# Optimization experiments

Measured on AMD Instinct MI355X. Metric: run time of the kernel, lower is better.

Reference implementation:

```python
import jax, jax.numpy as jnp
import numpy as np

B, S, HID = 1, 2048, 2048
NH = 16
D_NOPE, D_ROPE, D_V = 128, 64, 128
D_QK = D_NOPE + D_ROPE            # 192
KV_R = 512                        # kv_lora_rank
EPS = 1e-6
SCALING = D_QK ** -0.5
NEG = -1e9


def rms_norm(x, w):
    xf = x.astype(jnp.float32)
    var = jnp.mean(xf * xf, axis=-1, keepdims=True)
    return w * (xf * jax.lax.rsqrt(var + EPS)).astype(x.dtype)


def rotate_half(x):
    x1, x2 = jnp.split(x, 2, axis=-1)
    return jnp.concatenate([-x2, x1], axis=-1)


def deinterleave(x):
    # torch: view(..., d//2, 2).transpose(-1, -2).reshape(..., d)
    # => [x0, x2, x4, ..., x1, x3, x5, ...]
    return jnp.concatenate([x[..., 0::2], x[..., 1::2]], axis=-1)


def setup_inputs() -> dict:
    key = jax.random.key(0)
    ks = jax.random.split(key, 6)
    hidden_states = jax.random.normal(ks[0], (B, S, HID), jnp.float32)
    # rotary cos/sin over qk_rope_head_dim
    inv_freq = 1.0 / (10000.0 ** (np.arange(0, D_ROPE, 2, dtype=np.float32) / D_ROPE))
    freqs = np.outer(np.arange(S, dtype=np.float32), inv_freq)   # [S, D_ROPE/2]
    emb = np.concatenate([freqs, freqs], axis=-1)                # [S, D_ROPE]
    cos = jnp.asarray(np.cos(emb), jnp.float32)[None]            # [1, S, D_ROPE]
    sin = jnp.asarray(np.sin(emb), jnp.float32)[None]
    # additive causal mask [1, 1, S, S]
    causal = np.where(np.tril(np.ones((S, S), dtype=bool)), 0.0, NEG).astype(np.float32)
    attention_mask = jnp.asarray(causal)[None, None]
    sc = lambda k, shp: jax.random.normal(k, shp, jnp.float32) * (shp[-1] ** -0.5)
    q_proj_w = sc(ks[1], (NH * D_QK, HID))
    kv_a_proj_w = sc(ks[2], (KV_R + D_ROPE, HID))
    kv_a_ln_w = jnp.ones((KV_R,), jnp.float32)
    kv_b_proj_w = sc(ks[3], (NH * (D_NOPE + D_V), KV_R))
    o_proj_w = sc(ks[4], (HID, NH * D_V))
    return dict(hidden_states=hidden_states, cos=cos, sin=sin,
                attention_mask=attention_mask, q_proj_w=q_proj_w,
                kv_a_proj_w=kv_a_proj_w, kv_a_ln_w=kv_a_ln_w,
                kv_b_proj_w=kv_b_proj_w, o_proj_w=o_proj_w)


def reference(hidden_states, cos, sin, attention_mask,
              q_proj_w, kv_a_proj_w, kv_a_ln_w, kv_b_proj_w, o_proj_w):
    b, s, _ = hidden_states.shape
    # Q projection -> [b, NH, s, D_QK]
    q = (hidden_states @ q_proj_w.T).reshape(b, s, NH, D_QK).transpose(0, 2, 1, 3)
    q_pass, q_rot = q[..., :D_NOPE], q[..., D_NOPE:]
    # compressed KV + shared rope key
    ckv = hidden_states @ kv_a_proj_w.T                           # [b, s, KV_R + D_ROPE]
    k_pass_c, k_rot = ckv[..., :KV_R], ckv[..., KV_R:]
    kv = (rms_norm(k_pass_c, kv_a_ln_w) @ kv_b_proj_w.T)
    kv = kv.reshape(b, s, NH, D_NOPE + D_V).transpose(0, 2, 1, 3)  # [b, NH, s, .]
    k_pass, value_states = kv[..., :D_NOPE], kv[..., D_NOPE:]
    k_rot = k_rot.reshape(b, 1, s, D_ROPE)
    # interleaved RoPE (rope_interleave=True)
    q_rot = deinterleave(q_rot)
    k_rot = deinterleave(k_rot)
    c = cos[:, None]  # [1, 1, s, D_ROPE]
    sn = sin[:, None]
    q_rot = q_rot * c + rotate_half(q_rot) * sn
    k_rot = k_rot * c + rotate_half(k_rot) * sn
    k_rot = jnp.broadcast_to(k_rot, (b, NH, s, D_ROPE))
    query_states = jnp.concatenate([q_pass, q_rot], axis=-1)      # [b, NH, s, D_QK]
    key_states = jnp.concatenate([k_pass, k_rot], axis=-1)
    # eager attention (num_key_value_groups == 1)
    scores = jnp.einsum('bhqd,bhkd->bhqk', query_states, key_states) * SCALING
    scores = scores + attention_mask[:, :, :, :s]
    attn = jax.nn.softmax(scores.astype(jnp.float32), axis=-1).astype(query_states.dtype)
    attn_out = jnp.einsum('bhqk,bhkd->bhqd', attn, value_states)  # [b, NH, s, D_V]
    attn_out = attn_out.transpose(0, 2, 1, 3).reshape(b, s, NH * D_V)
    return attn_out @ o_proj_w.T
```

## Files before the change

kernel.cpp:

```cpp
#include <hip/hip_runtime.h>
#include <hip/hip_bf16.h>
#include <stdint.h>
#include <stddef.h>

#define S_LEN 2048
#define HID_DIM 2048
#define NH 16
#define D_QK 192
#define D_NOPE 128
#define D_ROPE 64
#define D_V 128
#define KV_R 512
#define CKV_N (KV_R + D_ROPE)
#define KVB_N (NH * (D_NOPE + D_V))
#define QN (NH * D_QK)
#define SCALING 0.07216878364870322f

typedef __attribute__((ext_vector_type(8))) short short8;
typedef __attribute__((ext_vector_type(4))) short short4v;
typedef __attribute__((ext_vector_type(4))) float f32x4;

__device__ __forceinline__ short f2bf_bits(float f) {
  unsigned u = __float_as_uint(f);
  unsigned r = (u + 0x7fffu + ((u >> 16) & 1u)) >> 16;
  return (short)(r & 0xffffu);
}
__device__ __forceinline__ float bf2f(short b) {
  return __uint_as_float(((unsigned)(unsigned short)b) << 16);
}

__device__ __forceinline__ f32x4 mfma_bf16(short8 a, short8 b, f32x4 c) {
  return __builtin_amdgcn_mfma_f32_16x16x32_bf16(a, b, c, 0, 0, 0);
}

__global__ __launch_bounds__(256)
void cvt_k(const float* __restrict__ in, short* __restrict__ out, int n4) {
  const int i = blockIdx.x * 256 + threadIdx.x;
  if (i >= n4) return;
  const float4 v = ((const float4*)in)[i];
  short4v o;
  o.x = f2bf_bits(v.x); o.y = f2bf_bits(v.y);
  o.z = f2bf_bits(v.z); o.w = f2bf_bits(v.w);
  ((short4v*)out)[i] = o;
}

template <bool OUTF32>
__global__ __launch_bounds__(256, 3)
void gemm_bt(const short* __restrict__ A, const short* __restrict__ B,
             void* __restrict__ Cv, int M, int N, int K) {
  __shared__ short sA[2][128 * 32];
  __shared__ short sB[2][128 * 32];
  const int tid  = threadIdx.x;
  const int wave = tid >> 6;
  const int lane = tid & 63;
  const int bm = blockIdx.y * 128;
  const int bn = blockIdx.x * 128;
  const int wr = wave >> 1, wc = wave & 1;
  const int fr = lane & 15, fk = (lane >> 4) * 8;
  const int srow = lane >> 2;
  const int scol = (lane & 3) * 8;

  f32x4 acc[4][4];
  for (int i = 0; i < 4; ++i)
    for (int j = 0; j < 4; ++j)
      for (int r = 0; r < 4; ++r) acc[i][j][r] = 0.f;

  for (int k0 = 0; k0 < K; k0 += 64) {
    __syncthreads();
#pragma unroll
    for (int cc = 0; cc < 2; ++cc) {
      const int c = wave * 2 + cc;
      const int ar = bm + c * 16 + srow;
      int br = bn + c * 16 + srow; if (br > N - 1) br = N - 1;
#pragma unroll
      for (int kh = 0; kh < 2; ++kh) {
        __builtin_amdgcn_global_load_lds(
            (const __attribute__((address_space(1))) void*)(A + (size_t)ar * K + k0 + kh * 32 + scol),
            (__attribute__((address_space(3))) void*)(sA[kh] + c * 512), 16, 0, 0);
        __builtin_amdgcn_global_load_lds(
            (const __attribute__((address_space(1))) void*)(B + (size_t)br * K + k0 + kh * 32 + scol),
            (__attribute__((address_space(3))) void*)(sB[kh] + c * 512), 16, 0, 0);
      }
    }
    __syncthreads();
#pragma unroll
    for (int kh = 0; kh < 2; ++kh) {
      short8 af[4], bfr[4];
#pragma unroll
      for (int i = 0; i < 4; ++i)
        af[i] = *(const short8*)(sA[kh] + (wr * 64 + i * 16 + fr) * 32 + fk);
#pragma unroll
      for (int j = 0; j < 4; ++j)
        bfr[j] = *(const short8*)(sB[kh] + (wc * 64 + j * 16 + fr) * 32 + fk);
#pragma unroll
      for (int i = 0; i < 4; ++i)
#pragma unroll
        for (int j = 0; j < 4; ++j)
          acc[i][j] = mfma_bf16(af[i], bfr[j], acc[i][j]);
    }
  }

  const int cr = (lane >> 4) * 4, ccol = lane & 15;
#pragma unroll
  for (int i = 0; i < 4; ++i)
#pragma unroll
    for (int j = 0; j < 4; ++j) {
      const int col = bn + wc * 64 + j * 16 + ccol;
      if (col < N) {
#pragma unroll
        for (int r = 0; r < 4; ++r) {
          const int row = bm + wr * 64 + i * 16 + cr + r;
          if (OUTF32)
            ((float*)Cv)[(size_t)row * N + col] = acc[i][j][r];
          else
            ((short*)Cv)[(size_t)row * N + col] = f2bf_bits(acc[i][j][r]);
        }
      }
    }
}

__global__ __launch_bounds__(256)
void rmsnorm_k(const short* __restrict__ ckv, const float* __restrict__ w,
               short* __restrict__ out) {
  const int s = blockIdx.x, t = threadIdx.x;
  const short* x = ckv + (size_t)s * CKV_N;
  float v0 = bf2f(x[2 * t]), v1 = bf2f(x[2 * t + 1]);
  float ss = v0 * v0 + v1 * v1;
#pragma unroll
  for (int off = 1; off < 64; off <<= 1) ss += __shfl_xor(ss, off, 64);
  __shared__ float red[4];
  if ((t & 63) == 0) red[t >> 6] = ss;
  __syncthreads();
  const float tot = red[0] + red[1] + red[2] + red[3];
  const float sc = rsqrtf(tot * (1.0f / 512.0f) + 1e-6f);
  out[(size_t)s * KV_R + 2 * t]     = f2bf_bits(v0 * sc * w[2 * t]);
  out[(size_t)s * KV_R + 2 * t + 1] = f2bf_bits(v1 * sc * w[2 * t + 1]);
}

__global__ __launch_bounds__(256)
void prep_k(const short* __restrict__ q, const short* __restrict__ ckv,
            const short* __restrict__ kvb, const float* __restrict__ cosb,
            const float* __restrict__ sinb,
            short* __restrict__ Qs, short* __restrict__ Ks) {
  const int s = blockIdx.x, t = threadIdx.x;
  __shared__ float cs[32], sn[32];
  __shared__ short krs[64];
  if (t < 32) {
    const float c  = cosb[(size_t)s * 64 + t];
    const float si = sinb[(size_t)s * 64 + t];
    cs[t] = c; sn[t] = si;
    const float e0 = bf2f(ckv[(size_t)s * CKV_N + KV_R + 2 * t]);
    const float e1 = bf2f(ckv[(size_t)s * CKV_N + KV_R + 2 * t + 1]);
    krs[t]      = f2bf_bits(e0 * c - e1 * si);
    krs[t + 32] = f2bf_bits(e1 * c + e0 * si);
  }
  __syncthreads();
  const int h = t >> 4, i = t & 15;
  *(short8*)(Qs + ((size_t)h * S_LEN + s) * D_QK + i * 8) =
      *(const short8*)(q + (size_t)s * QN + h * D_QK + i * 8);
  *(short8*)(Ks + ((size_t)h * S_LEN + s) * D_QK + i * 8) =
      *(const short8*)(kvb + (size_t)s * KVB_N + h * 256 + i * 8);
#pragma unroll
  for (int p = 0; p < 2; ++p) {
    const int ii = i * 2 + p;
    const float e0 = bf2f(q[(size_t)s * QN + h * D_QK + 128 + 2 * ii]);
    const float e1 = bf2f(q[(size_t)s * QN + h * D_QK + 128 + 2 * ii + 1]);
    Qs[((size_t)h * S_LEN + s) * D_QK + 128 + ii] = f2bf_bits(e0 * cs[ii] - e1 * sn[ii]);
    Qs[((size_t)h * S_LEN + s) * D_QK + 160 + ii] = f2bf_bits(e1 * cs[ii] + e0 * sn[ii]);
  }
#pragma unroll
  for (int p = 0; p < 4; ++p) {
    const int idx = t * 4 + p;
    const int hh = idx >> 6, ii = idx & 63;
    Ks[((size_t)hh * S_LEN + s) * D_QK + 128 + ii] = krs[ii];
  }
}

__global__ __launch_bounds__(256)
void vtr_k(const short* __restrict__ kvb, short* __restrict__ Vt) {
  const int st = blockIdx.x, dt = blockIdx.y, h = blockIdx.z;
  __shared__ short sT[64][72];
  const int id = threadIdx.x;
#pragma unroll
  for (int p = 0; p < 2; ++p) {
    const int q = id + p * 256;
    const int row = q >> 3, c8 = q & 7;
    *(short8*)(&sT[row][c8 * 8]) =
        *(const short8*)(kvb + (size_t)(st * 64 + row) * KVB_N + h * 256 + 128 + dt * 64 + c8 * 8);
  }
  __syncthreads();
#pragma unroll
  for (int p = 0; p < 2; ++p) {
    const int q = id + p * 256;
    const int drow = q >> 3, c8 = q & 7;
    short8 o;
#pragma unroll
    for (int j = 0; j < 8; ++j) o[j] = sT[c8 * 8 + j][drow];
    *(short8*)(Vt + ((size_t)h * D_V + dt * 64 + drow) * S_LEN + st * 64 + c8 * 8) = o;
  }
}

__global__ __launch_bounds__(256, 2)
void flash_k(const short* __restrict__ Qs, const short* __restrict__ Ks,
             const short* __restrict__ Vt, short* __restrict__ Oc) {
  __shared__ short sK[64 * 200];
  __shared__ short sVt[128 * 72];
  __shared__ short P_lds[4][16 * 72];
  const int tid = threadIdx.x;
  const int wv = tid >> 6;
  const int lane = tid & 63;
  const int blk = blockIdx.x;
  const int h = ((blk & 7) << 1) | ((blk >> 3) & 1);
  const int qb = 31 - (blk >> 4);
  const int q0 = qb * 64 + wv * 16;
  const int fr = lane & 15, g = lane >> 4;

  const short* Qh = Qs + (size_t)h * S_LEN * D_QK;
  const short* Kh = Ks + (size_t)h * S_LEN * D_QK;
  const short* Vh = Vt + (size_t)h * D_V * S_LEN;

  short8 qa[6];
#pragma unroll
  for (int c = 0; c < 6; ++c)
    qa[c] = *(const short8*)(Qh + (size_t)(q0 + fr) * D_QK + c * 32 + g * 8);

  f32x4 o[8];
  for (int f = 0; f < 8; ++f)
    for (int r = 0; r < 4; ++r) o[f][r] = 0.f;
  float m_i[4] = {-1e30f, -1e30f, -1e30f, -1e30f};
  float l_i[4] = {0.f, 0.f, 0.f, 0.f};

  short* pl = &P_lds[wv][0];
  const int jn = qb + 1;
  for (int jt = 0; jt < jn; ++jt) {
    const int j0 = jt << 6;
    __syncthreads();
    short8 kc[6], vc[4];
#pragma unroll
    for (int p = 0; p < 6; ++p) {
      const int id = tid + p * 256;
      const int row = id / 24, c8 = id % 24;
      kc[p] = *(const short8*)(Kh + (size_t)(j0 + row) * D_QK + c8 * 8);
    }
#pragma unroll
    for (int p = 0; p < 4; ++p) {
      const int id = tid + p * 256;
      const int row = id >> 3, c8 = id & 7;
      vc[p] = *(const short8*)(Vh + (size_t)row * S_LEN + j0 + c8 * 8);
    }
#pragma unroll
    for (int p = 0; p < 6; ++p) {
      const int id = tid + p * 256;
      const int row = id / 24, c8 = id % 24;
      *(short8*)(sK + row * 200 + c8 * 8) = kc[p];
    }
#pragma unroll
    for (int p = 0; p < 4; ++p) {
      const int id = tid + p * 256;
      const int row = id >> 3, c8 = id & 7;
      *(short8*)(sVt + row * 72 + c8 * 8) = vc[p];
    }
    __syncthreads();

    f32x4 sc[4];
#pragma unroll
    for (int t = 0; t < 4; ++t)
      for (int r = 0; r < 4; ++r) sc[t][r] = -1e30f;
#pragma unroll
    for (int t = 0; t < 4; ++t) {
      if (j0 + t * 16 <= q0 + 15) {
        f32x4 a;
        for (int r = 0; r < 4; ++r) a[r] = 0.f;
        const short* kr = sK + (t * 16 + fr) * 200 + g * 8;
#pragma unroll
        for (int c = 0; c < 6; ++c)
          a = mfma_bf16(qa[c], *(const short8*)(kr + c * 32), a);
        sc[t] = a;
      }
    }
    float tm[4];
#pragma unroll
    for (int r = 0; r < 4; ++r) {
      const int row = q0 + g * 4 + r;
      float mx = -1e30f;
#pragma unroll
      for (int t = 0; t < 4; ++t) {
        const float v = (j0 + t * 16 + fr <= row) ? sc[t][r] * SCALING : -1e30f;
        sc[t][r] = v;
        mx = fmaxf(mx, v);
      }
      tm[r] = mx;
    }
#pragma unroll
    for (int off = 1; off < 16; off <<= 1)
#pragma unroll
      for (int r = 0; r < 4; ++r)
        tm[r] = fmaxf(tm[r], __shfl_xor(tm[r], off, 16));
    float ps[4];
#pragma unroll
    for (int r = 0; r < 4; ++r) {
      const float mnew = fmaxf(m_i[r], tm[r]);
      const float alpha = __expf(m_i[r] - mnew);
      m_i[r] = mnew;
      l_i[r] *= alpha;
      float s = 0.f;
#pragma unroll
      for (int t = 0; t < 4; ++t) {
        const float p = __expf(sc[t][r] - mnew);
        sc[t][r] = p;
        s += p;
      }
      ps[r] = s;
#pragma unroll
      for (int f = 0; f < 8; ++f) o[f][r] *= alpha;
    }
#pragma unroll
    for (int off = 1; off < 16; off <<= 1)
#pragma unroll
      for (int r = 0; r < 4; ++r)
        ps[r] += __shfl_xor(ps[r], off, 16);
#pragma unroll
    for (int r = 0; r < 4; ++r) l_i[r] += ps[r];

#pragma unroll
    for (int r = 0; r < 4; ++r)
#pragma unroll
      for (int t = 0; t < 4; ++t)
        pl[(g * 4 + r) * 72 + t * 16 + fr] = f2bf_bits(sc[t][r]);
    __builtin_amdgcn_fence(__ATOMIC_ACQ_REL, "wavefront");
    const short8 pa0 = *(const short8*)(pl + fr * 72 + g * 8);
    const short8 pa1 = *(const short8*)(pl + fr * 72 + 32 + g * 8);

#pragma unroll
    for (int f = 0; f < 8; ++f) {
      const short* vr = sVt + (f * 16 + fr) * 72 + g * 8;
      const short8 vb0 = *(const short8*)(vr);
      const short8 vb1 = *(const short8*)(vr + 32);
      o[f] = mfma_bf16(pa1, vb1, mfma_bf16(pa0, vb0, o[f]));
    }
  }

#pragma unroll
  for (int r = 0; r < 4; ++r) {
    const float inv = 1.0f / l_i[r];
    const int row = q0 + g * 4 + r;
#pragma unroll
    for (int f = 0; f < 8; ++f)
      Oc[(size_t)row * (NH * D_V) + h * D_V + f * 16 + fr] = f2bf_bits(o[f][r] * inv);
  }
}

extern "C" void kernel_launch(void* const* d_in, const int* in_sizes, int n_in,
                              void* d_out, int out_size, void* d_ws, size_t ws_size,
                              hipStream_t stream) {
  const float* hidden = (const float*)d_in[0];
  const float* cosb   = (const float*)d_in[1];
  const float* sinb   = (const float*)d_in[2];
  const float* q_w    = (const float*)d_in[4];
  const float* kva_w  = (const float*)d_in[5];
  const float* ln_w   = (const float*)d_in[6];
  const float* kvb_w  = (const float*)d_in[7];
  const float* o_w    = (const float*)d_in[8];
  float* out = (float*)d_out;

  char* ws = (char*)d_ws;
  size_t off = 0;
  auto alloc = [&](size_t elems) {
    short* p = (short*)(ws + off);
    off += ((elems * 2 + 255) & ~(size_t)255);
    return p;
  };
  short* hid_b  = alloc((size_t)S_LEN * HID_DIM);
  short* q_wb   = alloc((size_t)QN * HID_DIM);
  short* kva_wb = alloc((size_t)CKV_N * HID_DIM);
  short* kvb_wb = alloc((size_t)KVB_N * KV_R);
  short* o_wb   = alloc((size_t)HID_DIM * NH * D_V);
  short* q    = alloc((size_t)S_LEN * QN);
  short* ckv  = alloc((size_t)S_LEN * CKV_N);
  short* ckvn = alloc((size_t)S_LEN * KV_R);
  short* kvb  = alloc((size_t)S_LEN * KVB_N);
  short* Qs   = alloc((size_t)NH * S_LEN * D_QK);
  short* Ks   = alloc((size_t)NH * S_LEN * D_QK);
  short* Vt   = alloc((size_t)NH * D_V * S_LEN);
  short* Oc   = alloc((size_t)S_LEN * NH * D_V);

  dim3 blk(256);
  auto cvt = [&](const float* src, short* dst, size_t n) {
    const int n4 = (int)(n / 4);
    cvt_k<<<dim3((n4 + 255) / 256), blk, 0, stream>>>(src, dst, n4);
  };
  cvt(hidden, hid_b, (size_t)S_LEN * HID_DIM);
  cvt(q_w,    q_wb,  (size_t)QN * HID_DIM);
  cvt(kva_w,  kva_wb,(size_t)CKV_N * HID_DIM);
  cvt(kvb_w,  kvb_wb,(size_t)KVB_N * KV_R);
  cvt(o_w,    o_wb,  (size_t)HID_DIM * NH * D_V);

  gemm_bt<false><<<dim3(QN / 128, S_LEN / 128), blk, 0, stream>>>(
      hid_b, q_wb, q, S_LEN, QN, HID_DIM);
  gemm_bt<false><<<dim3((CKV_N + 127) / 128, S_LEN / 128), blk, 0, stream>>>(
      hid_b, kva_wb, ckv, S_LEN, CKV_N, HID_DIM);
  rmsnorm_k<<<dim3(S_LEN), blk, 0, stream>>>(ckv, ln_w, ckvn);
  gemm_bt<false><<<dim3(KVB_N / 128, S_LEN / 128), blk, 0, stream>>>(
      ckvn, kvb_wb, kvb, S_LEN, KVB_N, KV_R);
  prep_k<<<dim3(S_LEN), blk, 0, stream>>>(q, ckv, kvb, cosb, sinb, Qs, Ks);
  vtr_k<<<dim3(S_LEN / 64, D_V / 64, NH), blk, 0, stream>>>(kvb, Vt);
  flash_k<<<dim3(NH * 128 / 4), blk, 0, stream>>>(Qs, Ks, Vt, Oc);
  gemm_bt<true><<<dim3(HID_DIM / 128, S_LEN / 128), blk, 0, stream>>>(
      Oc, o_wb, out, S_LEN, HID_DIM, NH * D_V);
}
```

Measured before the change: 360.6 us.

## Pair causal query tiles in flash kernel, fuse Q/KV-A GEMMs and converts

The flash kernel now gives each block two query tiles, a light one (a) and a heavy one (31-a). They share each K/V tile load, which balances causal work and halves the grid to 256 blocks. The Q and kv_a projections are concatenated into one GEMM with a combined output buffer. The five fp32→bf16 conversion launches are merged into one kernel. The changes cut launch count, K/V reloads and tail imbalance, at the cost of roughly double register pressure in flash and fewer blocks in flight.

```diff
diff --git a/kernel.cpp b/kernel.cpp
--- a/kernel.cpp
+++ b/kernel.cpp
@@ -14,6 +14,7 @@
 #define CKV_N (KV_R + D_ROPE)
 #define KVB_N (NH * (D_NOPE + D_V))
 #define QN (NH * D_QK)
+#define CAT_N (QN + CKV_N)
 #define SCALING 0.07216878364870322f
 
 typedef __attribute__((ext_vector_type(8))) short short8;
@@ -34,14 +35,25 @@
 }
 
 __global__ __launch_bounds__(256)
-void cvt_k(const float* __restrict__ in, short* __restrict__ out, int n4) {
+void cvt5_k(const float* __restrict__ s0, short* __restrict__ d0, int c0,
+            const float* __restrict__ s1, short* __restrict__ d1, int c1,
+            const float* __restrict__ s2, short* __restrict__ d2, int c2,
+            const float* __restrict__ s3, short* __restrict__ d3, int c3,
+            const float* __restrict__ s4, short* __restrict__ d4, int c4) {
   const int i = blockIdx.x * 256 + threadIdx.x;
-  if (i >= n4) return;
-  const float4 v = ((const float4*)in)[i];
+  const float* s; short* d; int base;
+  if      (i < c0) { s = s0; d = d0; base = 0;  }
+  else if (i < c1) { s = s1; d = d1; base = c0; }
+  else if (i < c2) { s = s2; d = d2; base = c1; }
+  else if (i < c3) { s = s3; d = d3; base = c2; }
+  else if (i < c4) { s = s4; d = d4; base = c3; }
+  else return;
+  const int j = i - base;
+  const float4 v = ((const float4*)s)[j];
   short4v o;
   o.x = f2bf_bits(v.x); o.y = f2bf_bits(v.y);
   o.z = f2bf_bits(v.z); o.w = f2bf_bits(v.w);
-  ((short4v*)out)[i] = o;
+  ((short4v*)d)[j] = o;
 }
 
 template <bool OUTF32>
@@ -120,10 +132,10 @@
 }
 
 __global__ __launch_bounds__(256)
-void rmsnorm_k(const short* __restrict__ ckv, const float* __restrict__ w,
+void rmsnorm_k(const short* __restrict__ qckv, const float* __restrict__ w,
                short* __restrict__ out) {
   const int s = blockIdx.x, t = threadIdx.x;
-  const short* x = ckv + (size_t)s * CKV_N;
+  const short* x = qckv + (size_t)s * CAT_N + QN;
   float v0 = bf2f(x[2 * t]), v1 = bf2f(x[2 * t + 1]);
   float ss = v0 * v0 + v1 * v1;
 #pragma unroll
@@ -138,33 +150,33 @@
 }
 
 __global__ __launch_bounds__(256)
-void prep_k(const short* __restrict__ q, const short* __restrict__ ckv,
-            const short* __restrict__ kvb, const float* __restrict__ cosb,
-            const float* __restrict__ sinb,
+void prep_k(const short* __restrict__ qckv, const short* __restrict__ kvb,
+            const float* __restrict__ cosb, const float* __restrict__ sinb,
             short* __restrict__ Qs, short* __restrict__ Ks) {
   const int s = blockIdx.x, t = threadIdx.x;
+  const short* qrow = qckv + (size_t)s * CAT_N;
   __shared__ float cs[32], sn[32];
   __shared__ short krs[64];
   if (t < 32) {
     const float c  = cosb[(size_t)s * 64 + t];
     const float si = sinb[(size_t)s * 64 + t];
     cs[t] = c; sn[t] = si;
-    const float e0 = bf2f(ckv[(size_t)s * CKV_N + KV_R + 2 * t]);
-    const float e1 = bf2f(ckv[(size_t)s * CKV_N + KV_R + 2 * t + 1]);
+    const float e0 = bf2f(qrow[QN + KV_R + 2 * t]);
+    const float e1 = bf2f(qrow[QN + KV_R + 2 * t + 1]);
     krs[t]      = f2bf_bits(e0 * c - e1 * si);
     krs[t + 32] = f2bf_bits(e1 * c + e0 * si);
   }
   __syncthreads();
   const int h = t >> 4, i = t & 15;
   *(short8*)(Qs + ((size_t)h * S_LEN + s) * D_QK + i * 8) =
-      *(const short8*)(q + (size_t)s * QN + h * D_QK + i * 8);
+      *(const short8*)(qrow + h * D_QK + i * 8);
   *(short8*)(Ks + ((size_t)h * S_LEN + s) * D_QK + i * 8) =
       *(const short8*)(kvb + (size_t)s * KVB_N + h * 256 + i * 8);
 #pragma unroll
   for (int p = 0; p < 2; ++p) {
     const int ii = i * 2 + p;
-    const float e0 = bf2f(q[(size_t)s * QN + h * D_QK + 128 + 2 * ii]);
-    const float e1 = bf2f(q[(size_t)s * QN + h * D_QK + 128 + 2 * ii + 1]);
+    const float e0 = bf2f(qrow[h * D_QK + 128 + 2 * ii]);
+    const float e1 = bf2f(qrow[h * D_QK + 128 + 2 * ii + 1]);
     Qs[((size_t)h * S_LEN + s) * D_QK + 128 + ii] = f2bf_bits(e0 * cs[ii] - e1 * sn[ii]);
     Qs[((size_t)h * S_LEN + s) * D_QK + 160 + ii] = f2bf_bits(e1 * cs[ii] + e0 * sn[ii]);
   }
@@ -211,29 +223,38 @@
   const int lane = tid & 63;
   const int blk = blockIdx.x;
   const int h = ((blk & 7) << 1) | ((blk >> 3) & 1);
-  const int qb = 31 - (blk >> 4);
-  const int q0 = qb * 64 + wv * 16;
+  const int a = blk >> 4;
+  const int b = 31 - a;
   const int fr = lane & 15, g = lane >> 4;
+  const int q0[2] = { a * 64 + wv * 16, b * 64 + wv * 16 };
 
   const short* Qh = Qs + (size_t)h * S_LEN * D_QK;
   const short* Kh = Ks + (size_t)h * S_LEN * D_QK;
   const short* Vh = Vt + (size_t)h * D_V * S_LEN;
 
-  short8 qa[6];
-#pragma unroll
-  for (int c = 0; c < 6; ++c)
-    qa[c] = *(const short8*)(Qh + (size_t)(q0 + fr) * D_QK + c * 32 + g * 8);
-
-  f32x4 o[8];
-  for (int f = 0; f < 8; ++f)
-    for (int r = 0; r < 4; ++r) o[f][r] = 0.f;
-  float m_i[4] = {-1e30f, -1e30f, -1e30f, -1e30f};
-  float l_i[4] = {0.f, 0.f, 0.f, 0.f};
+  short8 qa[2][6];
+#pragma unroll
+  for (int rt = 0; rt < 2; ++rt)
+#pragma unroll
+    for (int c = 0; c < 6; ++c)
+      qa[rt][c] = *(const short8*)(Qh + (size_t)(q0[rt] + fr) * D_QK + c * 32 + g * 8);
+
+  f32x4 o[2][8];
+  float m_i[2][4], l_i[2][4];
+#pragma unroll
+  for (int rt = 0; rt < 2; ++rt)
+#pragma unroll
+    for (int r = 0; r < 4; ++r) {
+      m_i[rt][r] = -1e30f; l_i[rt][r] = 0.f;
+#pragma unroll
+      for (int f = 0; f < 8; ++f) o[rt][f][r] = 0.f;
+    }
 
   short* pl = &P_lds[wv][0];
-  const int jn = qb + 1;
+  const int jn = b + 1;
   for (int jt = 0; jt < jn; ++jt) {
     const int j0 = jt << 6;
+    const bool lightOn = (jt <= a);
     __syncthreads();
     short8 kc[6], vc[4];
 #pragma unroll
@@ -262,92 +283,112 @@
     }
     __syncthreads();
 
-    f32x4 sc[4];
-#pragma unroll
-    for (int t = 0; t < 4; ++t)
-      for (int r = 0; r < 4; ++r) sc[t][r] = -1e30f;
+    f32x4 sc[2][4];
+#pragma unroll
+    for (int rt = 0; rt < 2; ++rt)
+#pragma unroll
+      for (int t = 0; t < 4; ++t)
+        for (int r = 0; r < 4; ++r) sc[rt][t][r] = -1e30f;
 #pragma unroll
     for (int t = 0; t < 4; ++t) {
-      if (j0 + t * 16 <= q0 + 15) {
-        f32x4 a;
-        for (int r = 0; r < 4; ++r) a[r] = 0.f;
-        const short* kr = sK + (t * 16 + fr) * 200 + g * 8;
+      const bool hOn = (j0 + t * 16 <= q0[1] + 15);
+      const bool lOn = lightOn && (j0 + t * 16 <= q0[0] + 15);
+      if (hOn || lOn) {
+        short8 kfr[6];
 #pragma unroll
         for (int c = 0; c < 6; ++c)
-          a = mfma_bf16(qa[c], *(const short8*)(kr + c * 32), a);
-        sc[t] = a;
-      }
-    }
-    float tm[4];
+          kfr[c] = *(const short8*)(sK + (t * 16 + fr) * 200 + c * 32 + g * 8);
+        if (lOn) {
+          f32x4 acc; for (int r = 0; r < 4; ++r) acc[r] = 0.f;
+#pragma unroll
+          for (int c = 0; c < 6; ++c) acc = mfma_bf16(qa[0][c], kfr[c], acc);
+          sc[0][t] = acc;
+        }
+        if (hOn) {
+          f32x4 acc; for (int r = 0; r < 4; ++r) acc[r] = 0.f;
+#pragma unroll
+          for (int c = 0; c < 6; ++c) acc = mfma_bf16(qa[1][c], kfr[c], acc);
+          sc[1][t] = acc;
+        }
+      }
+    }
+
+#pragma unroll
+    for (int rt = 0; rt < 2; ++rt) {
+      if (rt == 0 && !lightOn) continue;
+      const int qq = q0[rt];
+      float tm[4];
+#pragma unroll
+      for (int r = 0; r < 4; ++r) {
+        const int row = qq + g * 4 + r;
+        float mx = -1e30f;
+#pragma unroll
+        for (int t = 0; t < 4; ++t) {
+          const float v = (j0 + t * 16 + fr <= row) ? sc[rt][t][r] * SCALING : -1e30f;
+          sc[rt][t][r] = v;
+          mx = fmaxf(mx, v);
+        }
+        tm[r] = mx;
+      }
+#pragma unroll
+      for (int off = 1; off < 16; off <<= 1)
+#pragma unroll
+        for (int r = 0; r < 4; ++r)
+          tm[r] = fmaxf(tm[r], __shfl_xor(tm[r], off, 16));
+      float ps[4];
+#pragma unroll
+      for (int r = 0; r < 4; ++r) {
+        const float mnew = fmaxf(m_i[rt][r], tm[r]);
+        const float alpha = __expf(m_i[rt][r] - mnew);
+        m_i[rt][r] = mnew;
+        l_i[rt][r] *= alpha;
+        float s = 0.f;
+#pragma unroll
+        for (int t = 0; t < 4; ++t) {
+          const float p = __expf(sc[rt][t][r] - mnew);
+          sc[rt][t][r] = p;
+          s += p;
+        }
+        ps[r] = s;
+#pragma unroll
+        for (int f = 0; f < 8; ++f) o[rt][f][r] *= alpha;
+      }
+#pragma unroll
+      for (int off = 1; off < 16; off <<= 1)
+#pragma unroll
+        for (int r = 0; r < 4; ++r)
+          ps[r] += __shfl_xor(ps[r], off, 16);
+#pragma unroll
+      for (int r = 0; r < 4; ++r) l_i[rt][r] += ps[r];
+
+#pragma unroll
+      for (int r = 0; r < 4; ++r)
+#pragma unroll
+        for (int t = 0; t < 4; ++t)
+          pl[(g * 4 + r) * 72 + t * 16 + fr] = f2bf_bits(sc[rt][t][r]);
+      __builtin_amdgcn_fence(__ATOMIC_ACQ_REL, "wavefront");
+      const short8 pa0 = *(const short8*)(pl + fr * 72 + g * 8);
+      const short8 pa1 = *(const short8*)(pl + fr * 72 + 32 + g * 8);
+#pragma unroll
+      for (int f = 0; f < 8; ++f) {
+        const short* vr = sVt + (f * 16 + fr) * 72 + g * 8;
+        const short8 vb0 = *(const short8*)(vr);
+        const short8 vb1 = *(const short8*)(vr + 32);
+        o[rt][f] = mfma_bf16(pa1, vb1, mfma_bf16(pa0, vb0, o[rt][f]));
+      }
+    }
+  }
+
+#pragma unroll
+  for (int rt = 0; rt < 2; ++rt)
 #pragma unroll
     for (int r = 0; r < 4; ++r) {
-      const int row = q0 + g * 4 + r;
-      float mx = -1e30f;
-#pragma unroll
-      for (int t = 0; t < 4; ++t) {
-        const float v = (j0 + t * 16 + fr <= row) ? sc[t][r] * SCALING : -1e30f;
-        sc[t][r] = v;
-        mx = fmaxf(mx, v);
-      }
-      tm[r] = mx;
-    }
-#pragma unroll
-    for (int off = 1; off < 16; off <<= 1)
-#pragma unroll
-      for (int r = 0; r < 4; ++r)
-        tm[r] = fmaxf(tm[r], __shfl_xor(tm[r], off, 16));
-    float ps[4];
-#pragma unroll
-    for (int r = 0; r < 4; ++r) {
-      const float mnew = fmaxf(m_i[r], tm[r]);
-      const float alpha = __expf(m_i[r] - mnew);
-      m_i[r] = mnew;
-      l_i[r] *= alpha;
-      float s = 0.f;
-#pragma unroll
-      for (int t = 0; t < 4; ++t) {
-        const float p = __expf(sc[t][r] - mnew);
-        sc[t][r] = p;
-        s += p;
-      }
-      ps[r] = s;
-#pragma unroll
-      for (int f = 0; f < 8; ++f) o[f][r] *= alpha;
-    }
-#pragma unroll
-    for (int off = 1; off < 16; off <<= 1)
-#pragma unroll
-      for (int r = 0; r < 4; ++r)
-        ps[r] += __shfl_xor(ps[r], off, 16);
-#pragma unroll
-    for (int r = 0; r < 4; ++r) l_i[r] += ps[r];
-
-#pragma unroll
-    for (int r = 0; r < 4; ++r)
-#pragma unroll
-      for (int t = 0; t < 4; ++t)
-        pl[(g * 4 + r) * 72 + t * 16 + fr] = f2bf_bits(sc[t][r]);
-    __builtin_amdgcn_fence(__ATOMIC_ACQ_REL, "wavefront");
-    const short8 pa0 = *(const short8*)(pl + fr * 72 + g * 8);
-    const short8 pa1 = *(const short8*)(pl + fr * 72 + 32 + g * 8);
-
-#pragma unroll
-    for (int f = 0; f < 8; ++f) {
-      const short* vr = sVt + (f * 16 + fr) * 72 + g * 8;
-      const short8 vb0 = *(const short8*)(vr);
-      const short8 vb1 = *(const short8*)(vr + 32);
-      o[f] = mfma_bf16(pa1, vb1, mfma_bf16(pa0, vb0, o[f]));
-    }
-  }
-
-#pragma unroll
-  for (int r = 0; r < 4; ++r) {
-    const float inv = 1.0f / l_i[r];
-    const int row = q0 + g * 4 + r;
-#pragma unroll
-    for (int f = 0; f < 8; ++f)
-      Oc[(size_t)row * (NH * D_V) + h * D_V + f * 16 + fr] = f2bf_bits(o[f][r] * inv);
-  }
+      const float inv = 1.0f / l_i[rt][r];
+      const int row = q0[rt] + g * 4 + r;
+#pragma unroll
+      for (int f = 0; f < 8; ++f)
+        Oc[(size_t)row * (NH * D_V) + h * D_V + f * 16 + fr] = f2bf_bits(o[rt][f][r] * inv);
+    }
 }
 
 extern "C" void kernel_launch(void* const* d_in, const int* in_sizes, int n_in,
@@ -370,41 +411,40 @@
     off += ((elems * 2 + 255) & ~(size_t)255);
     return p;
   };
-  short* hid_b  = alloc((size_t)S_LEN * HID_DIM);
-  short* q_wb   = alloc((size_t)QN * HID_DIM);
-  short* kva_wb = alloc((size_t)CKV_N * HID_DIM);
-  short* kvb_wb = alloc((size_t)KVB_N * KV_R);
-  short* o_wb   = alloc((size_t)HID_DIM * NH * D_V);
-  short* q    = alloc((size_t)S_LEN * QN);
-  short* ckv  = alloc((size_t)S_LEN * CKV_N);
-  short* ckvn = alloc((size_t)S_LEN * KV_R);
-  short* kvb  = alloc((size_t)S_LEN * KVB_N);
-  short* Qs   = alloc((size_t)NH * S_LEN * D_QK);
-  short* Ks   = alloc((size_t)NH * S_LEN * D_QK);
-  short* Vt   = alloc((size_t)NH * D_V * S_LEN);
-  short* Oc   = alloc((size_t)S_LEN * NH * D_V);
+  short* hid_b   = alloc((size_t)S_LEN * HID_DIM);
+  short* qkva_wb = alloc((size_t)CAT_N * HID_DIM);
+  short* kvb_wb  = alloc((size_t)KVB_N * KV_R);
+  short* o_wb    = alloc((size_t)HID_DIM * NH * D_V);
+  short* qckv    = alloc((size_t)S_LEN * CAT_N);
+  short* ckvn    = alloc((size_t)S_LEN * KV_R);
+  short* kvb     = alloc((size_t)S_LEN * KVB_N);
+  short* Qs      = alloc((size_t)NH * S_LEN * D_QK);
+  short* Ks      = alloc((size_t)NH * S_LEN * D_QK);
+  short* Vt      = alloc((size_t)NH * D_V * S_LEN);
+  short* Oc      = alloc((size_t)S_LEN * NH * D_V);
 
   dim3 blk(256);
-  auto cvt = [&](const float* src, short* dst, size_t n) {
-    const int n4 = (int)(n / 4);
-    cvt_k<<<dim3((n4 + 255) / 256), blk, 0, stream>>>(src, dst, n4);
-  };
-  cvt(hidden, hid_b, (size_t)S_LEN * HID_DIM);
-  cvt(q_w,    q_wb,  (size_t)QN * HID_DIM);
-  cvt(kva_w,  kva_wb,(size_t)CKV_N * HID_DIM);
-  cvt(kvb_w,  kvb_wb,(size_t)KVB_N * KV_R);
-  cvt(o_w,    o_wb,  (size_t)HID_DIM * NH * D_V);
-
-  gemm_bt<false><<<dim3(QN / 128, S_LEN / 128), blk, 0, stream>>>(
-      hid_b, q_wb, q, S_LEN, QN, HID_DIM);
-  gemm_bt<false><<<dim3((CKV_N + 127) / 128, S_LEN / 128), blk, 0, stream>>>(
-      hid_b, kva_wb, ckv, S_LEN, CKV_N, HID_DIM);
-  rmsnorm_k<<<dim3(S_LEN), blk, 0, stream>>>(ckv, ln_w, ckvn);
+  const int n0 = (S_LEN * HID_DIM) / 4;
+  const int n1 = (QN * HID_DIM) / 4;
+  const int n2 = (CKV_N * HID_DIM) / 4;
+  const int n3 = (KVB_N * KV_R) / 4;
+  const int n4e = (HID_DIM * NH * D_V) / 4;
+  const int c0 = n0, c1 = c0 + n1, c2 = c1 + n2, c3 = c2 + n3, c4 = c3 + n4e;
+  cvt5_k<<<dim3((c4 + 255) / 256), blk, 0, stream>>>(
+      hidden, hid_b, c0,
+      q_w, qkva_wb, c1,
+      kva_w, qkva_wb + (size_t)QN * HID_DIM, c2,
+      kvb_w, kvb_wb, c3,
+      o_w, o_wb, c4);
+
+  gemm_bt<false><<<dim3((CAT_N + 127) / 128, S_LEN / 128), blk, 0, stream>>>(
+      hid_b, qkva_wb, qckv, S_LEN, CAT_N, HID_DIM);
+  rmsnorm_k<<<dim3(S_LEN), blk, 0, stream>>>(qckv, ln_w, ckvn);
   gemm_bt<false><<<dim3(KVB_N / 128, S_LEN / 128), blk, 0, stream>>>(
       ckvn, kvb_wb, kvb, S_LEN, KVB_N, KV_R);
-  prep_k<<<dim3(S_LEN), blk, 0, stream>>>(q, ckv, kvb, cosb, sinb, Qs, Ks);
+  prep_k<<<dim3(S_LEN), blk, 0, stream>>>(qckv, kvb, cosb, sinb, Qs, Ks);
   vtr_k<<<dim3(S_LEN / 64, D_V / 64, NH), blk, 0, stream>>>(kvb, Vt);
-  flash_k<<<dim3(NH * 128 / 4), blk, 0, stream>>>(Qs, Ks, Vt, Oc);
+  flash_k<<<dim3(NH * 16), blk, 0, stream>>>(Qs, Ks, Vt, Oc);
   gemm_bt<true><<<dim3(HID_DIM / 128, S_LEN / 128), blk, 0, stream>>>(
       Oc, o_wb, out, S_LEN, HID_DIM, NH * D_V);
 }
```

After: 320.1 us. 1.13x faster.
